# Kernel tuning notes

Hardware: AMD Instinct MI355X
Metric: run time of the kernel (lower is better)

## Reference

```python
import jax, jax.numpy as jnp
import numpy as np

N_NODES = 20000
N_EDGES = 160000
DIM = 64          # node embedding dim
SUB = 16          # sub_dim
NB = 5            # n_bonds_type
RB = 8            # radial basis size (FeNNol default)
CUTOFF = 5.0
NLAYERS = 3
HID = 64          # conv_hidden
NSPEC = 86        # species onehot size
XI_SHAPE = RB * SUB * NB   # 640
FC_IN = XI_SHAPE + SUB     # 656
LOG2 = float(np.log(2.0))


def ssp(x):
    # shifted softplus activation
    return jax.nn.softplus(x) - jnp.asarray(LOG2, x.dtype)


def radial_bessel(r):
    # sine Bessel radial basis on [0, cutoff]; r: [E] -> [E, RB]
    n = jnp.arange(1, RB + 1, dtype=r.dtype)
    x = r[:, None]
    return jnp.sqrt(jnp.asarray(2.0 / CUTOFF, r.dtype)) * jnp.sin(n * jnp.pi * x / CUTOFF) / x


def setup_inputs() -> dict:
    key = jax.random.key(0)
    ks = jax.random.split(key, 16)
    inp = {}
    inp['species'] = jax.random.randint(ks[0], (N_NODES,), 1, NSPEC, dtype=jnp.int32)
    inp['edge_src'] = jnp.sort(jax.random.randint(ks[1], (N_EDGES,), 0, N_NODES, dtype=jnp.int32))
    inp['edge_dst'] = jax.random.randint(ks[2], (N_EDGES,), 0, N_NODES, dtype=jnp.int32)
    # distances kept away from 0 to keep 1/r finite
    inp['distances'] = jax.random.uniform(ks[3], (N_EDGES,), jnp.float32, 0.5, CUTOFF)
    inp['switch'] = jax.random.uniform(ks[4], (N_EDGES,), jnp.float32)
    inp['bond_order'] = jax.random.uniform(ks[5], (N_EDGES, NB), jnp.float32)
    s = lambda fan: 1.0 / np.sqrt(fan)
    inp['W_species'] = jax.random.normal(ks[6], (NSPEC, DIM), jnp.float32) * s(NSPEC)
    inp['Wl'] = jax.random.normal(ks[7], (NLAYERS, DIM, 2 * SUB), jnp.float32) * s(DIM)
    inp['bl'] = jnp.zeros((NLAYERS, 2 * SUB), jnp.float32)
    inp['fcW1'] = jax.random.normal(ks[8], (NLAYERS, FC_IN, HID), jnp.float32) * s(FC_IN)
    inp['fcb1'] = jnp.zeros((NLAYERS, HID), jnp.float32)
    inp['fcW2'] = jax.random.normal(ks[9], (NLAYERS, HID, HID), jnp.float32) * s(HID)
    inp['fcb2'] = jnp.zeros((NLAYERS, HID), jnp.float32)
    inp['fcW3'] = jax.random.normal(ks[10], (NLAYERS, HID, DIM), jnp.float32) * s(HID)
    inp['fcb3'] = jnp.zeros((NLAYERS, DIM), jnp.float32)
    return inp


def reference(species, edge_src, edge_dst, distances, switch, bond_order,
              W_species, Wl, bl, fcW1, fcb1, fcW2, fcb2, fcW3, fcb3):
    # onehot(species) @ W (no bias) == embedding gather
    xi = W_species[species]                      # [N, DIM]
    rb = radial_bessel(distances)                # [E, RB]
    sw = switch[:, None]                         # [E, 1]
    for l in range(NLAYERS):
        h = xi @ Wl[l] + bl[l]                   # [N, 2*SUB]
        si, mi = h[:, :SUB], h[:, SUB:]
        # per-edge outer product: [E, RB, SUB, NB] -> [E, RB*SUB*NB]
        xi_j = (rb[:, :, None, None]
                * mi[edge_dst][:, None, :, None]
                * bond_order[:, None, None, :]).reshape(N_EDGES, XI_SHAPE)
        dxi = jax.ops.segment_sum(xi_j * sw, edge_src, num_segments=N_NODES)  # [N, 640]
        dxi = jnp.concatenate([dxi, si], axis=-1)                             # [N, 656]
        dxi = ssp(dxi @ fcW1[l] + fcb1[l])
        dxi = ssp(dxi @ fcW2[l] + fcb2[l])
        dxi = dxi @ fcW3[l] + fcb3[l]            # last FC layer linear
        xi = xi + dxi
    return xi
```

## Files before the change

### kernel.cpp

```cpp
#include <hip/hip_runtime.h>
#include <math.h>

#define N_NODES 20000
#define N_EDGES 160000
#define EPAD    160256
#define NGROUPS (EPAD / 8)
#define GSTRIDE 384
#define NTILES  1250

#define PI_F 3.14159265358979323846f
#define LN2_F 0.69314718055994530942f

#define W1PK 43008
#define W23PK 4096
#define WPK_LAYER 51200
#define XROW 680
#define CAP 312
#define NFILL_MAX 272

#define NW_EDGE 626
#define NW_XI   625
#define NW_PACK 600
#define NW_ROW  79
#define NW_TOTAL (NW_EDGE + NW_XI + NW_PACK + NW_ROW)

typedef short short8v __attribute__((ext_vector_type(8)));
typedef float f32x4 __attribute__((ext_vector_type(4)));
typedef unsigned short u16;
typedef unsigned long long ull;

__device__ __forceinline__ float sspf(float x) {
    return fmaxf(x, 0.0f) + log1pf(expf(-fabsf(x))) - LN2_F;
}
__device__ __forceinline__ u16 f2bf(float f) {
    unsigned int u = __float_as_uint(f);
    return (u16)((u + 0x7fffu + ((u >> 16) & 1u)) >> 16);
}
__device__ __forceinline__ unsigned int pk2(float a, float b) {
    return (unsigned int)f2bf(a) | ((unsigned int)f2bf(b) << 16);
}
__device__ __forceinline__ ull mge(int t) {
    t = t < 0 ? 0 : (t > 4 ? 4 : t);
    return t == 4 ? 0ULL : (~0ULL << (t * 16));
}

__device__ void edge_wt_work(int blk, const float* __restrict__ dist,
                             const float* __restrict__ sw,
                             const float* __restrict__ bo,
                             u16* __restrict__ WTg, char* smem)
{
    u16 (*tr)[264] = reinterpret_cast<u16(*)[264]>(smem);
    int tid = threadIdx.x;
    int e = blk * 256 + tid;

    if (e < N_EDGES) {
        float r = dist[e];
        float c = sqrtf(0.4f) / r * sw[e];
        float th = PI_F * r * 0.2f;
        float s1, c1;
        __sincosf(th, &s1, &c1);
        float k2c = 2.0f * c1;
        float rbv[8];
        rbv[0] = s1;
        float sp = 0.0f, sc = s1;
        #pragma unroll
        for (int n = 1; n < 8; ++n) {
            float sn = k2c * sc - sp;
            rbv[n] = sn;
            sp = sc; sc = sn;
        }
        #pragma unroll
        for (int n = 0; n < 8; ++n) rbv[n] *= c;
        float bov[5];
        #pragma unroll
        for (int b = 0; b < 5; ++b) bov[b] = bo[(size_t)e * 5 + b];
        #pragma unroll
        for (int n = 0; n < 8; ++n)
            #pragma unroll
            for (int b = 0; b < 5; ++b)
                tr[n * 5 + b][tid] = f2bf(rbv[n] * bov[b]);
    } else {
        #pragma unroll
        for (int j = 0; j < 40; ++j) tr[j][tid] = 0;
    }
    __syncthreads();

    #pragma unroll
    for (int i = 0; i < 6; ++i) {
        int r = i * 8 + (tid & 7);
        int gl = tid >> 3;
        uint4 v = make_uint4(0u, 0u, 0u, 0u);
        if (r < 40) v = *reinterpret_cast<const uint4*>(&tr[r][gl * 8]);
        *reinterpret_cast<uint4*>(
            WTg + ((size_t)(blk * 32 + gl) * GSTRIDE + r * 8)) = v;
    }
}

__device__ void row_start_work(int blk, const int* __restrict__ src,
                               int* __restrict__ row)
{
    int i = blk * 256 + threadIdx.x;
    if (i > N_NODES) return;
    int lo = 0, hi = N_EDGES;
    while (lo < hi) {
        int mid = (lo + hi) >> 1;
        if (src[mid] < i) lo = mid + 1; else hi = mid;
    }
    row[i] = lo;
}

__device__ void pack_w_work(int blk, const float* __restrict__ fcW1,
                            const float* __restrict__ fcW2,
                            const float* __restrict__ fcW3,
                            u16* __restrict__ Wpk)
{
    int idx = blk * 256 + threadIdx.x;
    if (idx >= 3 * WPK_LAYER) return;
    int layer = idx / WPK_LAYER;
    int r = idx - layer * WPK_LAYER;
    float val = 0.0f;
    if (r < W1PK) {
        int e = r;
        int j = e & 7, lane = (e >> 3) & 63, c16 = (e >> 9) & 3, ks = e >> 11;
        int k = ks * 32 + (lane >> 4) * 8 + j;
        int colm = c16 * 16 + (lane & 15);
        if (k < 640) {
            int nbv = k >> 4, ss = k & 15;
            int nn = nbv / 5, bb = nbv - nn * 5;
            val = fcW1[(size_t)layer * 656 * 64 + (size_t)(nn * 80 + ss * 5 + bb) * 64 + colm];
        } else if (k < 656) {
            val = fcW1[(size_t)layer * 656 * 64 + (size_t)k * 64 + colm];
        }
    } else {
        bool is2 = (r < W1PK + W23PK);
        const float* W = is2 ? fcW2 : fcW3;
        int e = is2 ? (r - W1PK) : (r - W1PK - W23PK);
        int j = e & 7, lane = (e >> 3) & 63, c16 = (e >> 9) & 3, ks = e >> 11;
        int k = ks * 32 + (lane >> 4) * 8 + j;
        int colm = c16 * 16 + (lane & 15);
        val = W[(size_t)layer * 64 * 64 + (size_t)k * 64 + colm];
    }
    Wpk[(size_t)layer * WPK_LAYER + r] = f2bf(val);
}

__device__ void xi_init_h_work(int blk, const int* __restrict__ species,
                               const float* __restrict__ Wsp,
                               const float* __restrict__ Wl0,
                               const float* __restrict__ bl0,
                               float* __restrict__ xi,
                               float* __restrict__ h, char* smem)
{
    float* xs = reinterpret_cast<float*>(smem);
    float* ws = reinterpret_cast<float*>(smem + 8192);
    int tid = threadIdx.x;
    int nb = blk * 32;

    #pragma unroll
    for (int i = 0; i < 2; ++i) {
        int idx = tid + i * 256;
        int node = idx >> 4, c4 = idx & 15;
        int sp = species[nb + node];
        float4 v = reinterpret_cast<const float4*>(Wsp + (size_t)sp * 64)[c4];
        reinterpret_cast<float4*>(xs)[idx] = v;
        reinterpret_cast<float4*>(xi)[(size_t)(nb + node) * 16 + c4] = v;
    }
    {
        const float4* wsrc = reinterpret_cast<const float4*>(Wl0);
        float4* wd = reinterpret_cast<float4*>(ws);
        #pragma unroll
        for (int i = 0; i < 2; ++i) wd[tid + i * 256] = wsrc[tid + i * 256];
    }
    __syncthreads();

    int c4g = tid & 7;
    int nrow = tid >> 3;
    float4 acc = *reinterpret_cast<const float4*>(bl0 + c4g * 4);
    const float* xr = xs + nrow * 64;
    #pragma unroll 8
    for (int j = 0; j < 64; ++j) {
        float xv = xr[j];
        float4 wv = *reinterpret_cast<const float4*>(ws + j * 32 + c4g * 4);
        acc.x = fmaf(xv, wv.x, acc.x);
        acc.y = fmaf(xv, wv.y, acc.y);
        acc.z = fmaf(xv, wv.z, acc.z);
        acc.w = fmaf(xv, wv.w, acc.w);
    }
    *reinterpret_cast<float4*>(h + (size_t)(nb + nrow) * 32 + c4g * 4) = acc;
}

__global__ __launch_bounds__(256) void setup_kernel(
    const float* __restrict__ dist, const float* __restrict__ sw,
    const float* __restrict__ bo, u16* __restrict__ WTg,
    const int* __restrict__ species, const float* __restrict__ Wsp,
    const float* __restrict__ Wl0, const float* __restrict__ bl0,
    float* __restrict__ xi, float* __restrict__ h0,
    const float* __restrict__ fcW1, const float* __restrict__ fcW2,
    const float* __restrict__ fcW3, u16* __restrict__ Wpk,
    const int* __restrict__ esrc, int* __restrict__ rowp)
{
    __shared__ __align__(16) char smem[21760];
    int wk = blockIdx.x;
    if (wk < NW_EDGE)
        edge_wt_work(wk, dist, sw, bo, WTg, smem);
    else if (wk < NW_EDGE + NW_XI)
        xi_init_h_work(wk - NW_EDGE, species, Wsp, Wl0, bl0, xi, h0, smem);
    else if (wk < NW_EDGE + NW_XI + NW_PACK)
        pack_w_work(wk - NW_EDGE - NW_XI, fcW1, fcW2, fcW3, Wpk);
    else
        row_start_work(wk - NW_EDGE - NW_XI - NW_PACK, esrc, rowp);
}

__global__ __launch_bounds__(256) void agg_fc_fused(
    const u16* __restrict__ WTg,
    const int* __restrict__ row,
    const int* __restrict__ dst,
    const float* __restrict__ h_in,
    float* __restrict__ h_out,
    const u16* __restrict__ Wpk,
    const float* __restrict__ b1,
    const float* __restrict__ b2,
    const float* __restrict__ b3,
    const float* __restrict__ Wl_next,
    const float* __restrict__ bl_next,
    int do_h,
    float* __restrict__ xi)
{
    __shared__ __align__(16) char smem[21760 + 16 * CAP * 2];
    u16 (*Xs)[XROW] = reinterpret_cast<u16(*)[XROW]>(smem);
    u16* mi  = reinterpret_cast<u16*>(smem + 21760);
    u16* Y1  = reinterpret_cast<u16*>(smem + 21760);
    u16* Y2  = reinterpret_cast<u16*>(smem + 21760 + 2304);
    float* Yo = reinterpret_cast<float*>(smem + 21760 + 4608);
    float* Wlds = reinterpret_cast<float*>(smem);
    float* Xn   = reinterpret_cast<float*>(smem + 8192);

    int tid = threadIdx.x;
    int wv = tid >> 6;
    int lane = tid & 63;
    int s = lane & 15;
    int kg = lane >> 4;
    int n0 = blockIdx.x * 16;
    int base = n0 + (wv << 2);

    int E0 = row[n0];
    int E1 = row[n0 + 16];
    int G0 = E0 & ~7;
    int nfill = E1 - G0;
    if (nfill > NFILL_MAX) nfill = NFILL_MAX;

    {
        int t = kg;
        u16* xr = &Xs[(wv << 2) + t][0];
        xr[640 + s] = f2bf(h_in[(size_t)(base + t) * 32 + s]);
        xr[656 + s] = 0;
    }

    for (int i = tid; i < nfill; i += 256) {
        int d = dst[G0 + i];
        const float4* hp = reinterpret_cast<const float4*>(h_in + (size_t)d * 32 + 16);
        float4 v0 = hp[0], v1 = hp[1], v2 = hp[2], v3 = hp[3];
        u16* col = mi + i;
        col[0 * CAP]  = f2bf(v0.x); col[1 * CAP]  = f2bf(v0.y);
        col[2 * CAP]  = f2bf(v0.z); col[3 * CAP]  = f2bf(v0.w);
        col[4 * CAP]  = f2bf(v1.x); col[5 * CAP]  = f2bf(v1.y);
        col[6 * CAP]  = f2bf(v1.z); col[7 * CAP]  = f2bf(v1.w);
        col[8 * CAP]  = f2bf(v2.x); col[9 * CAP]  = f2bf(v2.y);
        col[10 * CAP] = f2bf(v2.z); col[11 * CAP] = f2bf(v2.w);
        col[12 * CAP] = f2bf(v3.x); col[13 * CAP] = f2bf(v3.y);
        col[14 * CAP] = f2bf(v3.z); col[15 * CAP] = f2bf(v3.w);
    }
    __syncthreads();

    for (int t = 0; t < 4; ++t) {
        int node = base + t;
        int e0 = row[node], e1 = row[node + 1];
        int e0a = e0 & ~7;
        int L0 = e0a - G0;
        int nks = (e1 - e0a + 31) >> 5;

        f32x4 c0 = {0.f, 0.f, 0.f, 0.f};
        f32x4 c1 = {0.f, 0.f, 0.f, 0.f};
        f32x4 c2 = {0.f, 0.f, 0.f, 0.f};

        for (int kc = 0; kc < nks; ++kc) {
            int ebg = e0a + kc * 32 + kg * 8;
            int ebl = L0 + kc * 32 + kg * 8;
            uint4 bu = *reinterpret_cast<const uint4*>(mi + s * CAP + ebl);
            {
                int lo = e0 - ebg, hi = e1 - ebg;
                ull vA = mge(lo) & ~mge(hi);
                ull vB = mge(lo - 4) & ~mge(hi - 4);
                ull* bp = reinterpret_cast<ull*>(&bu);
                bp[0] &= vA;
                bp[1] &= vB;
            }
            short8v bfrag = *reinterpret_cast<short8v*>(&bu);
            const u16* gp = WTg + (size_t)(ebg >> 3) * GSTRIDE + (size_t)s * 8;
            short8v a0 = *reinterpret_cast<const short8v*>(gp);
            short8v a1 = *reinterpret_cast<const short8v*>(gp + 128);
            short8v a2 = *reinterpret_cast<const short8v*>(gp + 256);
            c0 = __builtin_amdgcn_mfma_f32_16x16x32_bf16(a0, bfrag, c0, 0, 0, 0);
            c1 = __builtin_amdgcn_mfma_f32_16x16x32_bf16(a1, bfrag, c1, 0, 0, 0);
            c2 = __builtin_amdgcn_mfma_f32_16x16x32_bf16(a2, bfrag, c2, 0, 0, 0);
        }

        u16* xr = &Xs[(wv << 2) + t][0];
        #pragma unroll
        for (int q = 0; q < 4; ++q) {
            xr[(kg * 4 + q) * 16 + s]      = f2bf(c0[q]);
            xr[(16 + kg * 4 + q) * 16 + s] = f2bf(c1[q]);
        }
        if (kg < 2) {
            #pragma unroll
            for (int q = 0; q < 4; ++q)
                xr[(32 + kg * 4 + q) * 16 + s] = f2bf(c2[q]);
        }
    }
    __syncthreads();

    int w = wv;
    int lrow = lane & 15;
    int lk = lane >> 4;
    int col = w * 16 + lrow;

    const u16* Wpk1 = Wpk;
    const u16* Wpk2 = Wpk + W1PK;
    const u16* Wpk3 = Wpk + W1PK + W23PK;

    f32x4 acc;
    {
        float bv = b1[col];
        acc[0] = bv; acc[1] = bv; acc[2] = bv; acc[3] = bv;
    }
    const u16* wp = Wpk1 + ((size_t)w * 64 + lane) * 8;
    #pragma unroll
    for (int ks = 0; ks < 21; ++ks) {
        short8v a = *reinterpret_cast<const short8v*>(&Xs[lrow][ks * 32 + lk * 8]);
        short8v b = *reinterpret_cast<const short8v*>(wp + (size_t)ks * 2048);
        acc = __builtin_amdgcn_mfma_f32_16x16x32_bf16(a, b, acc, 0, 0, 0);
    }
    __syncthreads();
    #pragma unroll
    for (int q = 0; q < 4; ++q)
        Y1[(lk * 4 + q) * 72 + col] = f2bf(sspf(acc[q]));
    __syncthreads();

    if (do_h) {
        const float4* wsrc = reinterpret_cast<const float4*>(Wl_next);
        float4* wd = reinterpret_cast<float4*>(Wlds);
        wd[tid] = wsrc[tid];
        wd[tid + 256] = wsrc[tid + 256];
    }

    {
        float bv = b2[col];
        acc[0] = bv; acc[1] = bv; acc[2] = bv; acc[3] = bv;
    }
    #pragma unroll
    for (int ks = 0; ks < 2; ++ks) {
        short8v a = *reinterpret_cast<const short8v*>(&Y1[lrow * 72 + ks * 32 + lk * 8]);
        short8v b = *reinterpret_cast<const short8v*>(Wpk2 + ((size_t)(ks * 4 + w) * 64 + lane) * 8);
        acc = __builtin_amdgcn_mfma_f32_16x16x32_bf16(a, b, acc, 0, 0, 0);
    }
    __syncthreads();
    #pragma unroll
    for (int q = 0; q < 4; ++q)
        Y2[(lk * 4 + q) * 72 + col] = f2bf(sspf(acc[q]));
    __syncthreads();

    {
        float bv = b3[col];
        acc[0] = bv; acc[1] = bv; acc[2] = bv; acc[3] = bv;
    }
    #pragma unroll
    for (int ks = 0; ks < 2; ++ks) {
        short8v a = *reinterpret_cast<const short8v*>(&Y2[lrow * 72 + ks * 32 + lk * 8]);
        short8v b = *reinterpret_cast<const short8v*>(Wpk3 + ((size_t)(ks * 4 + w) * 64 + lane) * 8);
        acc = __builtin_amdgcn_mfma_f32_16x16x32_bf16(a, b, acc, 0, 0, 0);
    }
    #pragma unroll
    for (int q = 0; q < 4; ++q)
        Yo[(lk * 4 + q) * 68 + col] = acc[q];
    __syncthreads();

    {
        int rr = tid >> 4;
        int cc = tid & 15;
        float4 dv = *reinterpret_cast<const float4*>(Yo + rr * 68 + cc * 4);
        float4* xpn = reinterpret_cast<float4*>(xi + (size_t)(n0 + rr) * 64 + cc * 4);
        float4 o = *xpn;
        o.x += dv.x; o.y += dv.y; o.z += dv.z; o.w += dv.w;
        *xpn = o;
        if (do_h)
            *reinterpret_cast<float4*>(Xn + rr * 68 + cc * 4) = o;
    }

    if (do_h) {
        __syncthreads();
        int node = tid >> 4;
        int c2 = (tid & 15) * 2;
        const float* xnr = Xn + node * 68;
        float h0 = bl_next[c2], h1 = bl_next[c2 + 1];
        #pragma unroll 8
        for (int j = 0; j < 64; ++j) {
            float xv = xnr[j];
            h0 = fmaf(xv, Wlds[j * 32 + c2], h0);
            h1 = fmaf(xv, Wlds[j * 32 + c2 + 1], h1);
        }
        *reinterpret_cast<float2*>(h_out + (size_t)(n0 + node) * 32 + c2) =
            make_float2(h0, h1);
    }
}

extern "C" void kernel_launch(void* const* d_in, const int* in_sizes, int n_in,
                              void* d_out, int out_size, void* d_ws, size_t ws_size,
                              hipStream_t stream) {
    const int*   species = (const int*)d_in[0];
    const int*   esrc    = (const int*)d_in[1];
    const int*   edst    = (const int*)d_in[2];
    const float* dist    = (const float*)d_in[3];
    const float* sw      = (const float*)d_in[4];
    const float* bo      = (const float*)d_in[5];
    const float* Wsp     = (const float*)d_in[6];
    const float* Wl      = (const float*)d_in[7];
    const float* bl      = (const float*)d_in[8];
    const float* fcW1    = (const float*)d_in[9];
    const float* fcb1    = (const float*)d_in[10];
    const float* fcW2    = (const float*)d_in[11];
    const float* fcb2    = (const float*)d_in[12];
    const float* fcW3    = (const float*)d_in[13];
    const float* fcb3    = (const float*)d_in[14];
    float* xi = (float*)d_out;

    char* ws = (char*)d_ws;
    u16*   WTg  = (u16*)ws;
    int*   rowp = (int*)(ws + 15384576);
    float* h0   = (float*)(ws + 15464704);
    float* h1   = (float*)(ws + 18024704);
    u16*   Wpk  = (u16*)(ws + 20584704);

    hipLaunchKernelGGL(setup_kernel, dim3(NW_TOTAL), dim3(256), 0, stream,
                       dist, sw, bo, WTg,
                       species, Wsp, Wl, bl, xi, h0,
                       fcW1, fcW2, fcW3, Wpk,
                       esrc, rowp);

    float* hbuf[2] = {h0, h1};
    for (int l = 0; l < 3; ++l) {
        int do_h = (l < 2) ? 1 : 0;
        int lnext = do_h ? (l + 1) : l;
        hipLaunchKernelGGL(agg_fc_fused, dim3(NTILES), dim3(256), 0, stream,
                           WTg, rowp, edst,
                           hbuf[l & 1], hbuf[(l + 1) & 1],
                           Wpk + (size_t)l * WPK_LAYER,
                           fcb1 + (size_t)l * 64, fcb2 + (size_t)l * 64,
                           fcb3 + (size_t)l * 64,
                           Wl + (size_t)lnext * 64 * 32,
                           bl + (size_t)lnext * 32,
                           do_h, xi);
    }
}
```

Before: 87.32 us.

## Shrink edge-weight row stride and compute next-layer projection with bf16 MFMA

Each edge-weight group row shrinks from 384 to 320 bf16 entries, so the zero padding rows are no longer stored. The third A-fragment is now loaded only for lanes holding real data and zero-filled for the rest, which cuts global traffic in the aggregation loop that runs for every layer. The per-tile node projection h = xi @ Wl for the next layer now uses bf16 MFMA on weights pre-packed in the setup kernel, replacing a scalar FMA loop over an LDS copy of fp32 weights. The cost is reduced precision in h, which is now computed from bf16-rounded xi and Wl, plus a small extra packing pass at setup.

```diff
diff --git a/kernel.cpp b/kernel.cpp
--- a/kernel.cpp
+++ b/kernel.cpp
@@ -5,7 +5,7 @@
 #define N_EDGES 160000
 #define EPAD    160256
 #define NGROUPS (EPAD / 8)
-#define GSTRIDE 384
+#define GSTRIDE 320
 #define NTILES  1250
 
 #define PI_F 3.14159265358979323846f
@@ -14,13 +14,14 @@
 #define W1PK 43008
 #define W23PK 4096
 #define WPK_LAYER 51200
+#define WLPK_LAYER 2048
 #define XROW 680
 #define CAP 312
 #define NFILL_MAX 272
 
 #define NW_EDGE 626
 #define NW_XI   625
-#define NW_PACK 600
+#define NW_PACK 616
 #define NW_ROW  79
 #define NW_TOTAL (NW_EDGE + NW_XI + NW_PACK + NW_ROW)
 
@@ -86,11 +87,10 @@
     __syncthreads();
 
     #pragma unroll
-    for (int i = 0; i < 6; ++i) {
+    for (int i = 0; i < 5; ++i) {
         int r = i * 8 + (tid & 7);
         int gl = tid >> 3;
-        uint4 v = make_uint4(0u, 0u, 0u, 0u);
-        if (r < 40) v = *reinterpret_cast<const uint4*>(&tr[r][gl * 8]);
+        uint4 v = *reinterpret_cast<const uint4*>(&tr[r][gl * 8]);
         *reinterpret_cast<uint4*>(
             WTg + ((size_t)(blk * 32 + gl) * GSTRIDE + r * 8)) = v;
     }
@@ -112,10 +112,25 @@
 __device__ void pack_w_work(int blk, const float* __restrict__ fcW1,
                             const float* __restrict__ fcW2,
                             const float* __restrict__ fcW3,
-                            u16* __restrict__ Wpk)
+                            const float* __restrict__ Wl,
+                            u16* __restrict__ Wpk,
+                            u16* __restrict__ Wlpk)
 {
     int idx = blk * 256 + threadIdx.x;
-    if (idx >= 3 * WPK_LAYER) return;
+    if (idx >= 3 * WPK_LAYER + 2 * WLPK_LAYER) return;
+    if (idx >= 3 * WPK_LAYER) {
+        int r2 = idx - 3 * WPK_LAYER;
+        int layer2 = r2 >> 11;
+        int e = r2 & 2047;
+        int j = e & 7, lane = (e >> 3) & 63;
+        int rest = e >> 9;
+        int ks = rest >> 1, cf = rest & 1;
+        int k = ks * 32 + (lane >> 4) * 8 + j;
+        int col = cf * 16 + (lane & 15);
+        Wlpk[(size_t)layer2 * WLPK_LAYER + e] =
+            f2bf(Wl[(size_t)(layer2 + 1) * 64 * 32 + (size_t)k * 32 + col]);
+        return;
+    }
     int layer = idx / WPK_LAYER;
     int r = idx - layer * WPK_LAYER;
     float val = 0.0f;
@@ -192,10 +207,11 @@
     const float* __restrict__ dist, const float* __restrict__ sw,
     const float* __restrict__ bo, u16* __restrict__ WTg,
     const int* __restrict__ species, const float* __restrict__ Wsp,
-    const float* __restrict__ Wl0, const float* __restrict__ bl0,
+    const float* __restrict__ Wl, const float* __restrict__ bl0,
     float* __restrict__ xi, float* __restrict__ h0,
     const float* __restrict__ fcW1, const float* __restrict__ fcW2,
     const float* __restrict__ fcW3, u16* __restrict__ Wpk,
+    u16* __restrict__ Wlpk,
     const int* __restrict__ esrc, int* __restrict__ rowp)
 {
     __shared__ __align__(16) char smem[21760];
@@ -203,9 +219,9 @@
     if (wk < NW_EDGE)
         edge_wt_work(wk, dist, sw, bo, WTg, smem);
     else if (wk < NW_EDGE + NW_XI)
-        xi_init_h_work(wk - NW_EDGE, species, Wsp, Wl0, bl0, xi, h0, smem);
+        xi_init_h_work(wk - NW_EDGE, species, Wsp, Wl, bl0, xi, h0, smem);
     else if (wk < NW_EDGE + NW_XI + NW_PACK)
-        pack_w_work(wk - NW_EDGE - NW_XI, fcW1, fcW2, fcW3, Wpk);
+        pack_w_work(wk - NW_EDGE - NW_XI, fcW1, fcW2, fcW3, Wl, Wpk, Wlpk);
     else
         row_start_work(wk - NW_EDGE - NW_XI - NW_PACK, esrc, rowp);
 }
@@ -220,7 +236,7 @@
     const float* __restrict__ b1,
     const float* __restrict__ b2,
     const float* __restrict__ b3,
-    const float* __restrict__ Wl_next,
+    const u16* __restrict__ Wlpk_l,
     const float* __restrict__ bl_next,
     int do_h,
     float* __restrict__ xi)
@@ -231,8 +247,7 @@
     u16* Y1  = reinterpret_cast<u16*>(smem + 21760);
     u16* Y2  = reinterpret_cast<u16*>(smem + 21760 + 2304);
     float* Yo = reinterpret_cast<float*>(smem + 21760 + 4608);
-    float* Wlds = reinterpret_cast<float*>(smem);
-    float* Xn   = reinterpret_cast<float*>(smem + 8192);
+    u16* Xnb  = reinterpret_cast<u16*>(smem + 8192);
 
     int tid = threadIdx.x;
     int wv = tid >> 6;
@@ -298,7 +313,9 @@
             const u16* gp = WTg + (size_t)(ebg >> 3) * GSTRIDE + (size_t)s * 8;
             short8v a0 = *reinterpret_cast<const short8v*>(gp);
             short8v a1 = *reinterpret_cast<const short8v*>(gp + 128);
-            short8v a2 = *reinterpret_cast<const short8v*>(gp + 256);
+            short8v a2 = {0, 0, 0, 0, 0, 0, 0, 0};
+            if (s < 8)
+                a2 = *reinterpret_cast<const short8v*>(gp + 256);
             c0 = __builtin_amdgcn_mfma_f32_16x16x32_bf16(a0, bfrag, c0, 0, 0, 0);
             c1 = __builtin_amdgcn_mfma_f32_16x16x32_bf16(a1, bfrag, c1, 0, 0, 0);
             c2 = __builtin_amdgcn_mfma_f32_16x16x32_bf16(a2, bfrag, c2, 0, 0, 0);
@@ -344,13 +361,6 @@
     for (int q = 0; q < 4; ++q)
         Y1[(lk * 4 + q) * 72 + col] = f2bf(sspf(acc[q]));
     __syncthreads();
-
-    if (do_h) {
-        const float4* wsrc = reinterpret_cast<const float4*>(Wl_next);
-        float4* wd = reinterpret_cast<float4*>(Wlds);
-        wd[tid] = wsrc[tid];
-        wd[tid + 256] = wsrc[tid + 256];
-    }
 
     {
         float bv = b2[col];
@@ -391,24 +401,34 @@
         float4 o = *xpn;
         o.x += dv.x; o.y += dv.y; o.z += dv.z; o.w += dv.w;
         *xpn = o;
-        if (do_h)
-            *reinterpret_cast<float4*>(Xn + rr * 68 + cc * 4) = o;
+        if (do_h) {
+            unsigned int* xb = reinterpret_cast<unsigned int*>(Xnb + rr * 64 + cc * 4);
+            xb[0] = pk2(o.x, o.y);
+            xb[1] = pk2(o.z, o.w);
+        }
     }
 
     if (do_h) {
         __syncthreads();
-        int node = tid >> 4;
-        int c2 = (tid & 15) * 2;
-        const float* xnr = Xn + node * 68;
-        float h0 = bl_next[c2], h1 = bl_next[c2 + 1];
-        #pragma unroll 8
-        for (int j = 0; j < 64; ++j) {
-            float xv = xnr[j];
-            h0 = fmaf(xv, Wlds[j * 32 + c2], h0);
-            h1 = fmaf(xv, Wlds[j * 32 + c2 + 1], h1);
-        }
-        *reinterpret_cast<float2*>(h_out + (size_t)(n0 + node) * 32 + c2) =
-            make_float2(h0, h1);
+        if (wv < 2) {
+            int cf = wv;
+            f32x4 hacc;
+            {
+                float bv = bl_next[cf * 16 + lrow];
+                hacc[0] = bv; hacc[1] = bv; hacc[2] = bv; hacc[3] = bv;
+            }
+            #pragma unroll
+            for (int ks = 0; ks < 2; ++ks) {
+                short8v a = *reinterpret_cast<const short8v*>(
+                    Xnb + lrow * 64 + ks * 32 + lk * 8);
+                short8v b = *reinterpret_cast<const short8v*>(
+                    Wlpk_l + ((size_t)(ks * 2 + cf) * 64 + lane) * 8);
+                hacc = __builtin_amdgcn_mfma_f32_16x16x32_bf16(a, b, hacc, 0, 0, 0);
+            }
+            #pragma unroll
+            for (int q = 0; q < 4; ++q)
+                h_out[(size_t)(n0 + lk * 4 + q) * 32 + cf * 16 + lrow] = hacc[q];
+        }
     }
 }
 
@@ -434,29 +454,29 @@
 
     char* ws = (char*)d_ws;
     u16*   WTg  = (u16*)ws;
-    int*   rowp = (int*)(ws + 15384576);
-    float* h0   = (float*)(ws + 15464704);
-    float* h1   = (float*)(ws + 18024704);
-    u16*   Wpk  = (u16*)(ws + 20584704);
+    int*   rowp = (int*)(ws + 12820480);
+    float* h0   = (float*)(ws + 12900608);
+    float* h1   = (float*)(ws + 15460608);
+    u16*   Wpk  = (u16*)(ws + 18020608);
+    u16*   Wlpk = (u16*)(ws + 18327808);
 
     hipLaunchKernelGGL(setup_kernel, dim3(NW_TOTAL), dim3(256), 0, stream,
                        dist, sw, bo, WTg,
                        species, Wsp, Wl, bl, xi, h0,
-                       fcW1, fcW2, fcW3, Wpk,
+                       fcW1, fcW2, fcW3, Wpk, Wlpk,
                        esrc, rowp);
 
     float* hbuf[2] = {h0, h1};
     for (int l = 0; l < 3; ++l) {
         int do_h = (l < 2) ? 1 : 0;
-        int lnext = do_h ? (l + 1) : l;
         hipLaunchKernelGGL(agg_fc_fused, dim3(NTILES), dim3(256), 0, stream,
                            WTg, rowp, edst,
                            hbuf[l & 1], hbuf[(l + 1) & 1],
                            Wpk + (size_t)l * WPK_LAYER,
                            fcb1 + (size_t)l * 64, fcb2 + (size_t)l * 64,
                            fcb3 + (size_t)l * 64,
-                           Wl + (size_t)lnext * 64 * 32,
-                           bl + (size_t)lnext * 32,
+                           Wlpk + (size_t)(do_h ? l : 0) * WLPK_LAYER,
+                           bl + (size_t)(l + (do_h ? 1 : 0)) * 32,
                            do_h, xi);
     }
 }
```

Result: faster. 84.11 us (-3.7%).
